# Kernel tuning notes

Measured on AMD Instinct MI355X. Metric: run time of the kernel, lower is better.

Reference implementation:

```python
import jax, jax.numpy as jnp
import numpy as np

B, L, E, H = 4, 4096, 1024, 16
DH = E // H          # 64 head dim
R, M, P = 1, 8, 16   # quadrature nodes, prf features, poly sketch dim
EPS = 1e-6
C = 2.0 + EPS


def setup_inputs() -> dict:
    key = jax.random.key(0)
    ks = jax.random.split(key, 10)
    x = jax.random.normal(ks[0], (B, L, E), dtype=jnp.float32)
    qkv_w = jax.random.normal(ks[1], (E, 3 * E), dtype=jnp.float32) * 0.02
    qkv_b = jnp.zeros((3 * E,), dtype=jnp.float32)
    out_w = jax.random.normal(ks[2], (E, E), dtype=jnp.float32) * 0.02
    out_b = jnp.zeros((E,), dtype=jnp.float32)
    omega = jax.random.normal(ks[3], (R, H, DH, M), dtype=jnp.float32)
    ts_hash1 = jax.random.randint(ks[4], (DH,), 0, P)
    ts_sign1 = jax.random.randint(ks[5], (DH,), 0, 2) * 2 - 1
    ts_hash2 = jax.random.randint(ks[6], (DH,), 0, P)
    ts_sign2 = jax.random.randint(ks[7], (DH,), 0, 2) * 2 - 1
    # laggauss(1): node=1.0, weight=1.0
    quad_nodes = jnp.array([1.0], dtype=jnp.float32) / C
    quad_weights = jnp.array([1.0], dtype=jnp.float32) / C
    return {"x": x, "qkv_w": qkv_w, "qkv_b": qkv_b, "out_w": out_w,
            "out_b": out_b, "omega": omega, "quad_nodes": quad_nodes,
            "quad_weights": quad_weights, "ts_hash1": ts_hash1,
            "ts_sign1": ts_sign1, "ts_hash2": ts_hash2, "ts_sign2": ts_sign2}


def _safe_normalize(x, eps=1e-6):
    norm = jnp.linalg.norm(x, axis=-1, keepdims=True)
    return x / jnp.clip(norm, eps)


def _count_sketch(x, h, s):
    # x: (B,H,L,DH); h,s: (DH,) int
    vals = x * s.astype(x.dtype)
    Mhot = jax.nn.one_hot(h, P, dtype=x.dtype)  # (DH, P)
    return jnp.dot(vals, Mhot)                  # (B,H,L,P)


def _poly_tensor_sketch(x, h1, s1, h2, s2):
    cs1 = _count_sketch(x, h1, s1)
    cs2 = _count_sketch(x, h2, s2)
    f1 = jnp.fft.rfft(cs1, axis=-1)
    f2 = jnp.fft.rfft(cs2, axis=-1)
    ts = jnp.fft.irfft(f1 * f2, n=P, axis=-1)
    return ts / jnp.sqrt(float(P))


def _prf_features(x, omega, quad_nodes):
    proj = jnp.einsum('bhld,rhdm->rbhlm', x, omega)
    s_vals = quad_nodes.reshape(-1, 1, 1, 1, 1)
    sqrt_2s = jnp.sqrt(2.0 * jnp.clip(s_vals, 0.0))
    exp_arg = jnp.clip(proj * sqrt_2s - s_vals, -10.0, 10.0)
    return jnp.exp(exp_arg) / jnp.sqrt(float(M))


def reference(x, qkv_w, qkv_b, out_w, out_b, omega, quad_nodes, quad_weights,
              ts_hash1, ts_sign1, ts_hash2, ts_sign2):
    qkv = x @ qkv_w + qkv_b
    q, k, v = jnp.split(qkv, 3, axis=-1)
    q = q.reshape(B, L, H, DH).transpose(0, 2, 1, 3)
    k = k.reshape(B, L, H, DH).transpose(0, 2, 1, 3)
    v = v.reshape(B, L, H, DH).transpose(0, 2, 1, 3)

    q_norm = _safe_normalize(q)
    k_norm = _safe_normalize(k)

    q_poly = _poly_tensor_sketch(q_norm, ts_hash1, ts_sign1, ts_hash2, ts_sign2)
    k_poly = _poly_tensor_sketch(k_norm, ts_hash1, ts_sign1, ts_hash2, ts_sign2)
    q_prf = _prf_features(q_norm, omega, quad_nodes)
    k_prf = _prf_features(k_norm, omega, quad_nodes)

    sq_w = jnp.sqrt(jnp.clip(quad_weights.reshape(-1, 1, 1, 1, 1), 0.0))
    q_prf = q_prf * sq_w
    k_prf = k_prf * sq_w

    q_fuse = jnp.einsum('bhlp,rbhlm->bhlrpm', q_poly, q_prf).reshape(B, H, L, -1)
    k_fuse = jnp.einsum('bhlp,rbhlm->bhlrpm', k_poly, k_prf).reshape(B, H, L, -1)

    kv = jnp.einsum('bhlf,bhld->bhfd', k_fuse, v)
    context = jnp.einsum('bhlf,bhfd->bhld', q_fuse, kv)
    k_sum = k_fuse.sum(axis=2)                              # (B,H,F)
    norm = jnp.einsum('bhlf,bhf->bhl', q_fuse, k_sum)
    output = context / jnp.clip(norm, 0.0001)[..., None]

    output = output.transpose(0, 2, 1, 3).reshape(B, L, E)
    return output @ out_w + out_b
```

## Files before the change

kernel.cpp:

```cpp
#include <hip/hip_runtime.h>

typedef unsigned short u16;
typedef __attribute__((ext_vector_type(8))) short bfrag8;
typedef __attribute__((ext_vector_type(4))) float f32x4;

__device__ __forceinline__ float b2f(u16 u){ union { unsigned ui; float f; } v; v.ui = ((unsigned)u) << 16; return v.f; }
__device__ __forceinline__ u16 f2b(float f){ union { float f; unsigned ui; } v; v.f = f; unsigned r = (v.ui + 0x7FFF + ((v.ui >> 16) & 1)) >> 16; return (u16)r; }

__device__ __forceinline__ void gl_lds16(const u16* g, u16* l){
  __builtin_amdgcn_global_load_lds(
      (const __attribute__((address_space(1))) unsigned*)g,
      (__attribute__((address_space(3))) unsigned*)l, 16, 0, 0);
}

__global__ __launch_bounds__(256) void zero_f32(float* p, int n){
  int i = blockIdx.x*256 + threadIdx.x;
  if (i < n) p[i] = 0.f;
}

__global__ __launch_bounds__(256) void split_x(const float* __restrict__ x,
    u16* __restrict__ xh, u16* __restrict__ xl){
  size_t i = ((size_t)blockIdx.x*256 + threadIdx.x) * 8;
  float v[8];
  *(float4*)v       = *(const float4*)(x + i);
  *(float4*)(v + 4) = *(const float4*)(x + i + 4);
  u16 h[8], l[8];
  #pragma unroll
  for (int j = 0; j < 8; ++j){ u16 a = f2b(v[j]); h[j] = a; l[j] = f2b(v[j] - b2f(a)); }
  *(uint4*)(xh + i) = *(uint4*)h;
  *(uint4*)(xl + i) = *(uint4*)l;
}

__global__ __launch_bounds__(256) void transpose_split(const float* __restrict__ W,
    u16* __restrict__ Th, u16* __restrict__ Tl, int K, int N){
  __shared__ float tile[32][33];
  int bx = blockIdx.x * 32, by = blockIdx.y * 32;
  int tx = threadIdx.x & 31, ty = threadIdx.x >> 5;
  #pragma unroll
  for (int i = 0; i < 32; i += 8) tile[ty+i][tx] = W[(size_t)(by+ty+i)*N + bx+tx];
  __syncthreads();
  #pragma unroll
  for (int i = 0; i < 32; i += 8){
    float v = tile[tx][ty+i];
    u16 h = f2b(v);
    Th[(size_t)(bx+ty+i)*K + by+tx] = h;
    Tl[(size_t)(bx+ty+i)*K + by+tx] = f2b(v - b2f(h));
  }
}

__global__ __launch_bounds__(256) void transpose_f2b(const float* __restrict__ W, u16* __restrict__ Wt, int K, int N){
  __shared__ u16 tile[32][33];
  int bx = blockIdx.x * 32, by = blockIdx.y * 32;
  int tx = threadIdx.x & 31, ty = threadIdx.x >> 5;
  #pragma unroll
  for (int i = 0; i < 32; i += 8) tile[ty+i][tx] = f2b(W[(size_t)(by+ty+i)*N + bx+tx]);
  __syncthreads();
  #pragma unroll
  for (int i = 0; i < 32; i += 8) Wt[(size_t)(bx+ty+i)*K + by+tx] = tile[tx][ty+i];
}

template<int NPROD>
__global__ __launch_bounds__(256) void gemm_planes(
    const u16* __restrict__ Ah, const u16* __restrict__ Al, int lda,
    const u16* __restrict__ Bh, const u16* __restrict__ Bl, int bn_off,
    const float* __restrict__ bias,
    float* __restrict__ Cq, float* __restrict__ Ck, u16* __restrict__ Cv, int K)
{
  constexpr int NS = (NPROD==3) ? 2 : 1;
  __shared__ __align__(16) u16 As[NS*4096];
  __shared__ __align__(16) u16 Bs[NS*4096];
  int tid = threadIdx.x, lane = tid & 63, wave = tid >> 6;
  int wm = wave >> 1, wn = wave & 1;
  int bm = blockIdx.y * 128, bn = blockIdx.x * 128;
  f32x4 acc[4][4];
  #pragma unroll
  for (int i=0;i<4;i++)
    #pragma unroll
    for (int j=0;j<4;j++)
      #pragma unroll
      for (int r=0;r<4;r++) acc[i][j][r] = 0.f;
  int mr = lane & 15, g = lane >> 4;
  int srow = (wave & 1)*64 + lane;
  int kc1 = (wave >> 1)*8;
  int kc2 = kc1 + 16;
  const u16* gA0 = Ah + (size_t)(bm + srow)*lda;
  const u16* gA1 = Al + (size_t)(bm + srow)*lda;
  const u16* gB0 = Bh + (size_t)(bn_off + bn + srow)*K;
  const u16* gB1 = Bl + (size_t)(bn_off + bn + srow)*K;
  u16* dA1 = &As[wave*512];  u16* dA2 = &As[(wave+4)*512];
  u16* dB1 = &Bs[wave*512];  u16* dB2 = &Bs[(wave+4)*512];

  for (int k0 = 0; k0 < K; k0 += 32) {
    gl_lds16(gA0 + k0 + kc1, dA1);
    gl_lds16(gA0 + k0 + kc2, dA2);
    gl_lds16(gB0 + k0 + kc1, dB1);
    gl_lds16(gB0 + k0 + kc2, dB2);
    if constexpr (NS > 1){
      gl_lds16(gA1 + k0 + kc1, dA1 + 4096);
      gl_lds16(gA1 + k0 + kc2, dA2 + 4096);
      gl_lds16(gB1 + k0 + kc1, dB1 + 4096);
      gl_lds16(gB1 + k0 + kc2, dB2 + 4096);
    }
    __syncthreads();
    bfrag8 af[NS][4], bf[NS][4];
    #pragma unroll
    for (int s=0;s<NS;s++){
      #pragma unroll
      for (int i=0;i<4;i++) af[s][i] = *(const bfrag8*)(&As[s*4096 + g*1024 + (wm*64 + i*16 + mr)*8]);
      #pragma unroll
      for (int j=0;j<4;j++) bf[s][j] = *(const bfrag8*)(&Bs[s*4096 + g*1024 + (wn*64 + j*16 + mr)*8]);
    }
#define MM(sa,sb) \
    { _Pragma("unroll") for (int i=0;i<4;i++){ _Pragma("unroll") for (int j=0;j<4;j++){ \
        acc[i][j] = __builtin_amdgcn_mfma_f32_16x16x32_bf16(af[sa][i], bf[sb][j], acc[i][j], 0, 0, 0); } } }
    if constexpr (NPROD == 3){ MM(0,1) MM(1,0) }
    MM(0,0)
#undef MM
    __syncthreads();
  }
  #pragma unroll
  for (int i=0;i<4;i++){
    #pragma unroll
    for (int j=0;j<4;j++){
      int col = bn_off + bn + wn*64 + j*16 + (lane & 15);
      float bv = bias[col];
      #pragma unroll
      for (int r=0;r<4;r++){
        int row = bm + wm*64 + i*16 + (lane>>4)*4 + r;
        float val = acc[i][j][r] + bv;
        if (col < 1024)      Cq[(size_t)row*1024 + col]        = val;
        else if (col < 2048) Ck[(size_t)row*1024 + (col-1024)] = val;
        else                 Cv[(size_t)row*1024 + (col-2048)] = f2b(val);
      }
    }
  }
}

__global__ __launch_bounds__(256) void gemm_b16(const u16* __restrict__ A, int lda,
    const u16* __restrict__ Bt, const float* __restrict__ bias, float* __restrict__ C, int N, int K)
{
  __shared__ __align__(16) u16 As[4096];
  __shared__ __align__(16) u16 Bs[4096];
  int tid = threadIdx.x, lane = tid & 63, wave = tid >> 6;
  int wm = wave >> 1, wn = wave & 1;
  int bm = blockIdx.y * 128, bn = blockIdx.x * 128;
  f32x4 acc[4][4];
  #pragma unroll
  for (int i=0;i<4;i++)
    #pragma unroll
    for (int j=0;j<4;j++)
      #pragma unroll
      for (int r=0;r<4;r++) acc[i][j][r] = 0.f;
  int mr = lane & 15, g = lane >> 4;
  int srow = (wave & 1)*64 + lane;
  int kc1 = (wave >> 1)*8, kc2 = kc1 + 16;
  const u16* gA = A  + (size_t)(bm + srow)*lda;
  const u16* gB = Bt + (size_t)(bn + srow)*K;
  u16* dA1 = &As[wave*512];  u16* dA2 = &As[(wave+4)*512];
  u16* dB1 = &Bs[wave*512];  u16* dB2 = &Bs[(wave+4)*512];
  for (int k0 = 0; k0 < K; k0 += 32) {
    gl_lds16(gA + k0 + kc1, dA1);
    gl_lds16(gA + k0 + kc2, dA2);
    gl_lds16(gB + k0 + kc1, dB1);
    gl_lds16(gB + k0 + kc2, dB2);
    __syncthreads();
    bfrag8 af[4], bf[4];
    #pragma unroll
    for (int i=0;i<4;i++) af[i] = *(const bfrag8*)(&As[g*1024 + (wm*64 + i*16 + mr)*8]);
    #pragma unroll
    for (int j=0;j<4;j++) bf[j] = *(const bfrag8*)(&Bs[g*1024 + (wn*64 + j*16 + mr)*8]);
    #pragma unroll
    for (int i=0;i<4;i++)
      #pragma unroll
      for (int j=0;j<4;j++)
        acc[i][j] = __builtin_amdgcn_mfma_f32_16x16x32_bf16(af[i], bf[j], acc[i][j], 0, 0, 0);
    __syncthreads();
  }
  #pragma unroll
  for (int i=0;i<4;i++){
    #pragma unroll
    for (int j=0;j<4;j++){
      int col = bn + wn*64 + j*16 + (lane & 15);
      float bv = bias[col];
      #pragma unroll
      for (int r=0;r<4;r++){
        int row = bm + wm*64 + i*16 + (lane>>4)*4 + r;
        C[(size_t)row*N + col] = acc[i][j][r] + bv;
      }
    }
  }
}

struct __align__(16) ConsT { int b1; float sg1; int b2; float sg2; };

#define FEATS_COMPUTE(TILE, TOKA)                                                \
  float sq = 0.f;                                                                \
  _Pragma("unroll")                                                              \
  for (int dd = 0; dd < 16; ++dd){ float u = TILE[(TOKA)*65 + g*16 + dd]; sq += u*u; } \
  sq += __shfl_xor(sq, 16); sq += __shfl_xor(sq, 32);                            \
  float sc = 1.f / fmaxf(sqrtf(sq), 1e-6f);                                      \
  float cs1[16], cs2[16], pm[8];                                                 \
  _Pragma("unroll") for (int p=0;p<16;p++){ cs1[p]=0.f; cs2[p]=0.f; }            \
  _Pragma("unroll") for (int m=0;m<8;m++) pm[m]=0.f;                             \
  _Pragma("unroll")                                                              \
  for (int dd = 0; dd < 16; ++dd){                                               \
    int d = g*16 + dd;                                                           \
    float un = TILE[(TOKA)*65 + d] * sc;                                         \
    ConsT cc = cons[d];                                                          \
    float v1 = un*cc.sg1, v2 = un*cc.sg2;                                        \
    _Pragma("unroll")                                                            \
    for (int p=0;p<16;p++){ cs1[p] += (cc.b1==p)?v1:0.f; cs2[p] += (cc.b2==p)?v2:0.f; } \
    _Pragma("unroll")                                                            \
    for (int m=0;m<8;m++) pm[m] += un * oms[d*8 + m];                            \
  }                                                                              \
  _Pragma("unroll")                                                              \
  for (int p=0;p<16;p++){ cs1[p] += __shfl_xor(cs1[p],16); cs1[p] += __shfl_xor(cs1[p],32); \
                          cs2[p] += __shfl_xor(cs2[p],16); cs2[p] += __shfl_xor(cs2[p],32); } \
  _Pragma("unroll")                                                              \
  for (int m=0;m<8;m++){ pm[m] += __shfl_xor(pm[m],16); pm[m] += __shfl_xor(pm[m],32); } \
  float poly4[4];                                                                \
  _Pragma("unroll")                                                              \
  for (int pi=0;pi<4;pi++){ int p = g*4 + pi; float s = 0.f;                     \
    _Pragma("unroll") for (int a=0;a<16;a++) s += cs1[a]*cs2[(p-a)&15];          \
    poly4[pi] = s * 0.25f; }                                                     \
  float prf[8];                                                                  \
  _Pragma("unroll")                                                              \
  for (int m=0;m<8;m++){ float e = fminf(fmaxf(pm[m]*sqrt2s - s_node, -10.f), 10.f); \
    prf[m] = expf(e) * pscale; }

__global__ __launch_bounds__(256) void kfeat_kv(const float* __restrict__ kf, const u16* __restrict__ vb,
    const float* __restrict__ omega, const float* __restrict__ qn, const float* __restrict__ qw,
    const int* __restrict__ h1, const int* __restrict__ s1,
    const int* __restrict__ h2, const int* __restrict__ s2,
    float* __restrict__ kvT, float* __restrict__ ksum)
{
  __shared__ float ktile[64*65];
  __shared__ __align__(16) u16 vtile[64*64];
  __shared__ __align__(16) u16 featT[128*72];
  __shared__ float oms[64*8];
  __shared__ ConsT cons[64];
  int tid = threadIdx.x, lane = tid & 63, wave = tid >> 6;
  int bh = blockIdx.y, b = bh >> 4, h = bh & 15;
  int chunk = blockIdx.x;
  if (tid < 64) {
    ConsT c; c.b1 = h1[tid]; c.sg1 = (float)s1[tid]; c.b2 = h2[tid]; c.sg2 = (float)s2[tid];
    cons[tid] = c;
  }
  for (int i = tid; i < 512; i += 256) oms[i] = omega[h*512 + i];
  float s_node = qn[0];
  float sqrt2s = sqrtf(2.f * fmaxf(s_node, 0.f));
  float pscale = 0.35355339059327373f * sqrtf(fmaxf(qw[0], 0.f));
  int tloc = lane & 15, g = lane >> 4;
  int tokA = wave*16 + tloc;
  int wm = wave >> 1, wn = wave & 1;
  int mr = lane & 15, kq8 = (lane >> 4) * 8;
  f32x4 acc[4][2];
  #pragma unroll
  for (int i=0;i<4;i++)
    #pragma unroll
    for (int jn=0;jn<2;jn++)
      #pragma unroll
      for (int r=0;r<4;r++) acc[i][jn][r] = 0.f;
  float kacc[32];
  #pragma unroll
  for (int j=0;j<32;j++) kacc[j] = 0.f;
  for (int sub = 0; sub < 8; ++sub) {
    int base = chunk*512 + sub*64;
    __syncthreads();
    for (int idx = tid; idx < 4096; idx += 256) {
      int t = idx >> 6, d = idx & 63;
      ktile[t*65 + d] = kf[(size_t)(b*4096 + base + t)*1024 + h*64 + d];
    }
    for (int slot = tid; slot < 512; slot += 256) {
      int t = slot >> 3, o = (slot & 7) * 8;
      *(uint4*)(&vtile[t*64 + o]) = *(const uint4*)(&vb[(size_t)(b*4096 + base + t)*1024 + h*64 + o]);
    }
    __syncthreads();
    {
      FEATS_COMPUTE(ktile, tokA)
      #pragma unroll
      for (int pi=0;pi<4;pi++){
        #pragma unroll
        for (int m=0;m<8;m++){
          int f = (g*4 + pi)*8 + m;
          float v = poly4[pi]*prf[m];
          featT[f*72 + tokA] = f2b(v);
          v += __shfl_xor(v,1); v += __shfl_xor(v,2); v += __shfl_xor(v,4); v += __shfl_xor(v,8);
          if (tloc == 0) kacc[pi*8 + m] += v;
        }
      }
    }
    __syncthreads();
    #pragma unroll
    for (int k0 = 0; k0 < 64; k0 += 32) {
      bfrag8 af[4];
      #pragma unroll
      for (int i=0;i<4;i++) af[i] = *(const bfrag8*)(&featT[(wm*64 + i*16 + mr)*72 + k0 + kq8]);
      #pragma unroll
      for (int jn=0;jn<2;jn++){
        int d = wn*32 + jn*16 + mr;
        short tmp[8];
        #pragma unroll
        for (int j=0;j<8;j++) tmp[j] = (short)vtile[(k0 + kq8 + j)*64 + d];
        bfrag8 bf = *(bfrag8*)tmp;
        #pragma unroll
        for (int i=0;i<4;i++)
          acc[i][jn] = __builtin_amdgcn_mfma_f32_16x16x32_bf16(af[i], bf, acc[i][jn], 0, 0, 0);
      }
    }
  }
  #pragma unroll
  for (int i=0;i<4;i++){
    #pragma unroll
    for (int jn=0;jn<2;jn++){
      int d = wn*32 + jn*16 + (lane & 15);
      #pragma unroll
      for (int r=0;r<4;r++){
        int f = wm*64 + i*16 + (lane>>4)*4 + r;
        atomicAdd(&kvT[((size_t)bh*64 + d)*128 + f], acc[i][jn][r]);
      }
    }
  }
  if (tloc == 0){
    #pragma unroll
    for (int j=0;j<32;j++) atomicAdd(&ksum[bh*128 + g*32 + j], kacc[j]);
  }
}

__global__ __launch_bounds__(256) void qfeat_ctx(const float* __restrict__ qf,
    const float* __restrict__ omega, const float* __restrict__ qn, const float* __restrict__ qw,
    const int* __restrict__ h1, const int* __restrict__ s1,
    const int* __restrict__ h2, const int* __restrict__ s2,
    const float* __restrict__ kvT, const float* __restrict__ ksum,
    u16* __restrict__ attn)
{
  __shared__ float qtile[64*65];
  __shared__ __align__(16) u16 feat[64*136];
  __shared__ __align__(16) u16 kvsb0[64*136];
  __shared__ __align__(16) u16 kvsb1[64*136];
  __shared__ float ksums[128];
  __shared__ float nrm_s[64];
  __shared__ float oms[64*8];
  __shared__ ConsT cons[64];
  int tid = threadIdx.x, lane = tid & 63, wave = tid >> 6;
  int bh = blockIdx.y, b = bh >> 4, h = bh & 15;
  int chunk = blockIdx.x;
  if (tid < 64) {
    ConsT c; c.b1 = h1[tid]; c.sg1 = (float)s1[tid]; c.b2 = h2[tid]; c.sg2 = (float)s2[tid];
    cons[tid] = c;
  }
  for (int i = tid; i < 512; i += 256) oms[i] = omega[h*512 + i];
  for (int idx = tid; idx < 8192; idx += 256) {
    int d = idx >> 7, f = idx & 127;
    float v = kvT[((size_t)bh*64 + d)*128 + f];
    u16 b0 = f2b(v);
    kvsb0[d*136 + f] = b0;
    kvsb1[d*136 + f] = f2b(v - b2f(b0));
  }
  if (tid < 128) ksums[tid] = ksum[bh*128 + tid];
  float s_node = qn[0];
  float sqrt2s = sqrtf(2.f * fmaxf(s_node, 0.f));
  float pscale = 0.35355339059327373f * sqrtf(fmaxf(qw[0], 0.f));
  int tloc = lane & 15, g = lane >> 4;
  int tokA = wave*16 + tloc;
  int mr = lane & 15, kq8 = (lane >> 4) * 8;
  for (int sub = 0; sub < 8; ++sub) {
    int base = chunk*512 + sub*64;
    for (int idx = tid; idx < 4096; idx += 256) {
      int t = idx >> 6, d = idx & 63;
      qtile[t*65 + d] = qf[(size_t)(b*4096 + base + t)*1024 + h*64 + d];
    }
    __syncthreads();
    {
      FEATS_COMPUTE(qtile, tokA)
      float nv = 0.f;
      #pragma unroll
      for (int pi=0;pi<4;pi++){
        #pragma unroll
        for (int m=0;m<8;m++){
          int f = (g*4 + pi)*8 + m;
          float v = poly4[pi]*prf[m];
          feat[tokA*136 + f] = f2b(v);
          nv += v * ksums[f];
        }
      }
      nv += __shfl_xor(nv, 16); nv += __shfl_xor(nv, 32);
      if (lane < 16) nrm_s[tokA] = nv;
    }
    __syncthreads();
    f32x4 cacc[4];
    #pragma unroll
    for (int jn=0;jn<4;jn++)
      #pragma unroll
      for (int r=0;r<4;r++) cacc[jn][r] = 0.f;
    #pragma unroll
    for (int k0 = 0; k0 < 128; k0 += 32) {
      bfrag8 af = *(const bfrag8*)(&feat[(wave*16 + mr)*136 + k0 + kq8]);
      #pragma unroll
      for (int jn=0;jn<4;jn++){
        int d = jn*16 + mr;
        bfrag8 b0 = *(const bfrag8*)(&kvsb0[d*136 + k0 + kq8]);
        cacc[jn] = __builtin_amdgcn_mfma_f32_16x16x32_bf16(af, b0, cacc[jn], 0, 0, 0);
        bfrag8 b1 = *(const bfrag8*)(&kvsb1[d*136 + k0 + kq8]);
        cacc[jn] = __builtin_amdgcn_mfma_f32_16x16x32_bf16(af, b1, cacc[jn], 0, 0, 0);
      }
    }
    #pragma unroll
    for (int jn=0;jn<4;jn++){
      int d = jn*16 + (lane & 15);
      #pragma unroll
      for (int r=0;r<4;r++){
        int row = (lane>>4)*4 + r;
        float nrm = nrm_s[wave*16 + row];
        int tok = base + wave*16 + row;
        attn[(size_t)(b*4096 + tok)*2048 + h*64 + d] = f2b(cacc[jn][r] / fmaxf(nrm, 1e-4f));
      }
    }
  }
}

extern "C" void kernel_launch(void* const* d_in, const int* in_sizes, int n_in,
                              void* d_out, int out_size, void* d_ws, size_t ws_size,
                              hipStream_t stream)
{
  const float* x     = (const float*)d_in[0];
  const float* qkv_w = (const float*)d_in[1];
  const float* qkv_b = (const float*)d_in[2];
  const float* out_w = (const float*)d_in[3];
  const float* out_b = (const float*)d_in[4];
  const float* omega = (const float*)d_in[5];
  const float* qn    = (const float*)d_in[6];
  const float* qw    = (const float*)d_in[7];
  const int* h1 = (const int*)d_in[8];
  const int* s1 = (const int*)d_in[9];
  const int* h2 = (const int*)d_in[10];
  const int* s2 = (const int*)d_in[11];

  const size_t SZ_Q  = (size_t)16384*1024*4;
  const size_t SZ_K  = (size_t)16384*1024*4;
  const size_t SZ_V  = (size_t)16384*1024*2;
  const size_t SZ_XH = (size_t)16384*1024*2;
  const size_t SZ_XL = (size_t)16384*1024*2;
  const size_t SZ_WH = (size_t)3072*1024*2;
  const size_t SZ_WL = (size_t)3072*1024*2;
  const size_t SZ_W2 = (size_t)1024*1024*2;
  const size_t SZ_KV = (size_t)64*64*128*4;
  char* ws = (char*)d_ws;
  float* qf  = (float*)ws;
  float* kf  = (float*)(ws + SZ_Q);
  u16*   vb  = (u16*)  (ws + SZ_Q + SZ_K);
  u16*   xh  = (u16*)  (ws + SZ_Q + SZ_K + SZ_V);
  u16*   xl  = (u16*)  (ws + SZ_Q + SZ_K + SZ_V + SZ_XH);
  u16*   wTh = (u16*)  (ws + SZ_Q + SZ_K + SZ_V + SZ_XH + SZ_XL);
  u16*   wTl = (u16*)  (ws + SZ_Q + SZ_K + SZ_V + SZ_XH + SZ_XL + SZ_WH);
  u16*   wT2 = (u16*)  (ws + SZ_Q + SZ_K + SZ_V + SZ_XH + SZ_XL + SZ_WH + SZ_WL);
  float* kvT = (float*)(ws + SZ_Q + SZ_K + SZ_V + SZ_XH + SZ_XL + SZ_WH + SZ_WL + SZ_W2);
  float* ksp = (float*)(ws + SZ_Q + SZ_K + SZ_V + SZ_XH + SZ_XL + SZ_WH + SZ_WL + SZ_W2 + SZ_KV);

  int nz = (int)((SZ_KV + (size_t)64*128*4) / 4);
  zero_f32<<<(nz+255)/256, 256, 0, stream>>>(kvT, nz);
  split_x<<<(16384*1024/8)/256, 256, 0, stream>>>(x, xh, xl);
  transpose_split<<<dim3(3072/32, 1024/32), 256, 0, stream>>>(qkv_w, wTh, wTl, 1024, 3072);
  transpose_f2b<<<dim3(1024/32, 1024/32), 256, 0, stream>>>(out_w, wT2, 1024, 1024);
  gemm_planes<3><<<dim3(16, 128), 256, 0, stream>>>(xh, xl, 1024, wTh, wTl, 0, qkv_b, qf, kf, vb, 1024);
  gemm_planes<1><<<dim3(8, 128), 256, 0, stream>>>(xh, xl, 1024, wTh, wTl, 2048, qkv_b, qf, kf, vb, 1024);
  kfeat_kv<<<dim3(8, 64), 256, 0, stream>>>(kf, vb, omega, qn, qw, h1, s1, h2, s2, kvT, ksp);
  qfeat_ctx<<<dim3(8, 64), 256, 0, stream>>>(qf, omega, qn, qw, h1, s1, h2, s2, kvT, ksp, (u16*)kf);
  gemm_b16<<<dim3(8, 128), 256, 0, stream>>>((const u16*)kf, 2048, wT2, out_b, (float*)d_out, 1024, 1024);
}
```

Measured before the change: 991.0 us.

## Double-buffer LDS tiles in both GEMM kernels to overlap loads with MFMA

Both GEMM kernels now use two LDS buffers per operand. The global-to-LDS load for the next 32-wide K slice is issued before the MFMA compute on the current slice, so the loop does two slices per iteration and one barrier per slice. The goal is to hide global memory latency behind matrix math. The cost is double the LDS per block, which may lower occupancy, and the loop now assumes K is a multiple of 64.

```diff
diff --git a/kernel.cpp b/kernel.cpp
--- a/kernel.cpp
+++ b/kernel.cpp
@@ -67,8 +67,8 @@
     float* __restrict__ Cq, float* __restrict__ Ck, u16* __restrict__ Cv, int K)
 {
   constexpr int NS = (NPROD==3) ? 2 : 1;
-  __shared__ __align__(16) u16 As[NS*4096];
-  __shared__ __align__(16) u16 Bs[NS*4096];
+  __shared__ __align__(16) u16 As[2*NS*4096];
+  __shared__ __align__(16) u16 Bs[2*NS*4096];
   int tid = threadIdx.x, lane = tid & 63, wave = tid >> 6;
   int wm = wave >> 1, wn = wave & 1;
   int bm = blockIdx.y * 128, bn = blockIdx.x * 128;
@@ -87,37 +87,49 @@
   const u16* gA1 = Al + (size_t)(bm + srow)*lda;
   const u16* gB0 = Bh + (size_t)(bn_off + bn + srow)*K;
   const u16* gB1 = Bl + (size_t)(bn_off + bn + srow)*K;
-  u16* dA1 = &As[wave*512];  u16* dA2 = &As[(wave+4)*512];
-  u16* dB1 = &Bs[wave*512];  u16* dB2 = &Bs[(wave+4)*512];
-
-  for (int k0 = 0; k0 < K; k0 += 32) {
-    gl_lds16(gA0 + k0 + kc1, dA1);
-    gl_lds16(gA0 + k0 + kc2, dA2);
-    gl_lds16(gB0 + k0 + kc1, dB1);
-    gl_lds16(gB0 + k0 + kc2, dB2);
-    if constexpr (NS > 1){
-      gl_lds16(gA1 + k0 + kc1, dA1 + 4096);
-      gl_lds16(gA1 + k0 + kc2, dA2 + 4096);
-      gl_lds16(gB1 + k0 + kc1, dB1 + 4096);
-      gl_lds16(gB1 + k0 + kc2, dB2 + 4096);
-    }
-    __syncthreads();
-    bfrag8 af[NS][4], bf[NS][4];
-    #pragma unroll
-    for (int s=0;s<NS;s++){
-      #pragma unroll
-      for (int i=0;i<4;i++) af[s][i] = *(const bfrag8*)(&As[s*4096 + g*1024 + (wm*64 + i*16 + mr)*8]);
-      #pragma unroll
-      for (int j=0;j<4;j++) bf[s][j] = *(const bfrag8*)(&Bs[s*4096 + g*1024 + (wn*64 + j*16 + mr)*8]);
-    }
-#define MM(sa,sb) \
+  u16* As0 = As;  u16* As1 = As + NS*4096;
+  u16* Bs0 = Bs;  u16* Bs1 = Bs + NS*4096;
+
+#define STG_P(AD, BD, KO) { \
+    gl_lds16(gA0 + (KO) + kc1, (AD) + wave*512); \
+    gl_lds16(gA0 + (KO) + kc2, (AD) + (wave+4)*512); \
+    gl_lds16(gB0 + (KO) + kc1, (BD) + wave*512); \
+    gl_lds16(gB0 + (KO) + kc2, (BD) + (wave+4)*512); \
+    if constexpr (NS > 1){ \
+      gl_lds16(gA1 + (KO) + kc1, (AD) + 4096 + wave*512); \
+      gl_lds16(gA1 + (KO) + kc2, (AD) + 4096 + (wave+4)*512); \
+      gl_lds16(gB1 + (KO) + kc1, (BD) + 4096 + wave*512); \
+      gl_lds16(gB1 + (KO) + kc2, (BD) + 4096 + (wave+4)*512); } }
+
+#define MMACC(sa,sb) \
     { _Pragma("unroll") for (int i=0;i<4;i++){ _Pragma("unroll") for (int j=0;j<4;j++){ \
         acc[i][j] = __builtin_amdgcn_mfma_f32_16x16x32_bf16(af[sa][i], bf[sb][j], acc[i][j], 0, 0, 0); } } }
-    if constexpr (NPROD == 3){ MM(0,1) MM(1,0) }
-    MM(0,0)
-#undef MM
-    __syncthreads();
-  }
+
+#define CMP_P(AS, BS) { \
+    bfrag8 af[NS][4], bf[NS][4]; \
+    _Pragma("unroll") \
+    for (int s=0;s<NS;s++){ \
+      _Pragma("unroll") \
+      for (int i=0;i<4;i++) af[s][i] = *(const bfrag8*)((AS) + s*4096 + g*1024 + (wm*64 + i*16 + mr)*8); \
+      _Pragma("unroll") \
+      for (int j=0;j<4;j++) bf[s][j] = *(const bfrag8*)((BS) + s*4096 + g*1024 + (wn*64 + j*16 + mr)*8); } \
+    if constexpr (NPROD == 3){ MMACC(0,1) MMACC(1,0) } \
+    MMACC(0,0) }
+
+  STG_P(As0, Bs0, 0)
+  __syncthreads();
+  for (int k0 = 0; k0 < K; k0 += 64) {
+    STG_P(As1, Bs1, k0 + 32)
+    CMP_P(As0, Bs0)
+    __syncthreads();
+    if (k0 + 64 < K) { STG_P(As0, Bs0, k0 + 64) }
+    CMP_P(As1, Bs1)
+    __syncthreads();
+  }
+#undef STG_P
+#undef CMP_P
+#undef MMACC
+
   #pragma unroll
   for (int i=0;i<4;i++){
     #pragma unroll
@@ -139,8 +151,8 @@
 __global__ __launch_bounds__(256) void gemm_b16(const u16* __restrict__ A, int lda,
     const u16* __restrict__ Bt, const float* __restrict__ bias, float* __restrict__ C, int N, int K)
 {
-  __shared__ __align__(16) u16 As[4096];
-  __shared__ __align__(16) u16 Bs[4096];
+  __shared__ __align__(16) u16 As[2*4096];
+  __shared__ __align__(16) u16 Bs[2*4096];
   int tid = threadIdx.x, lane = tid & 63, wave = tid >> 6;
   int wm = wave >> 1, wn = wave & 1;
   int bm = blockIdx.y * 128, bn = blockIdx.x * 128;
@@ -156,26 +168,40 @@
   int kc1 = (wave >> 1)*8, kc2 = kc1 + 16;
   const u16* gA = A  + (size_t)(bm + srow)*lda;
   const u16* gB = Bt + (size_t)(bn + srow)*K;
-  u16* dA1 = &As[wave*512];  u16* dA2 = &As[(wave+4)*512];
-  u16* dB1 = &Bs[wave*512];  u16* dB2 = &Bs[(wave+4)*512];
-  for (int k0 = 0; k0 < K; k0 += 32) {
-    gl_lds16(gA + k0 + kc1, dA1);
-    gl_lds16(gA + k0 + kc2, dA2);
-    gl_lds16(gB + k0 + kc1, dB1);
-    gl_lds16(gB + k0 + kc2, dB2);
-    __syncthreads();
-    bfrag8 af[4], bf[4];
-    #pragma unroll
-    for (int i=0;i<4;i++) af[i] = *(const bfrag8*)(&As[g*1024 + (wm*64 + i*16 + mr)*8]);
-    #pragma unroll
-    for (int j=0;j<4;j++) bf[j] = *(const bfrag8*)(&Bs[g*1024 + (wn*64 + j*16 + mr)*8]);
-    #pragma unroll
-    for (int i=0;i<4;i++)
-      #pragma unroll
-      for (int j=0;j<4;j++)
-        acc[i][j] = __builtin_amdgcn_mfma_f32_16x16x32_bf16(af[i], bf[j], acc[i][j], 0, 0, 0);
-    __syncthreads();
-  }
+  u16* As0 = As;  u16* As1 = As + 4096;
+  u16* Bs0 = Bs;  u16* Bs1 = Bs + 4096;
+
+#define STG_B(AD, BD, KO) { \
+    gl_lds16(gA + (KO) + kc1, (AD) + wave*512); \
+    gl_lds16(gA + (KO) + kc2, (AD) + (wave+4)*512); \
+    gl_lds16(gB + (KO) + kc1, (BD) + wave*512); \
+    gl_lds16(gB + (KO) + kc2, (BD) + (wave+4)*512); }
+
+#define CMP_B(AS, BS) { \
+    bfrag8 af[4], bf[4]; \
+    _Pragma("unroll") \
+    for (int i=0;i<4;i++) af[i] = *(const bfrag8*)((AS) + g*1024 + (wm*64 + i*16 + mr)*8); \
+    _Pragma("unroll") \
+    for (int j=0;j<4;j++) bf[j] = *(const bfrag8*)((BS) + g*1024 + (wn*64 + j*16 + mr)*8); \
+    _Pragma("unroll") \
+    for (int i=0;i<4;i++){ \
+      _Pragma("unroll") \
+      for (int j=0;j<4;j++) \
+        acc[i][j] = __builtin_amdgcn_mfma_f32_16x16x32_bf16(af[i], bf[j], acc[i][j], 0, 0, 0); } }
+
+  STG_B(As0, Bs0, 0)
+  __syncthreads();
+  for (int k0 = 0; k0 < K; k0 += 64) {
+    STG_B(As1, Bs1, k0 + 32)
+    CMP_B(As0, Bs0)
+    __syncthreads();
+    if (k0 + 64 < K) { STG_B(As0, Bs0, k0 + 64) }
+    CMP_B(As1, Bs1)
+    __syncthreads();
+  }
+#undef STG_B
+#undef CMP_B
+
   #pragma unroll
   for (int i=0;i<4;i++){
     #pragma unroll
```

After: 1.117 ms. +12.7%, slower.
